# Optimization experiments

Hardware: AMD Instinct MI355X
Metric: run time of the kernel (lower is better)

The kernel has to match this reference:

```python
import jax, jax.numpy as jnp
import numpy as np

N_USERS = 200000
N_ITEMS = 100000
N_NODES = N_USERS + N_ITEMS
N_EDGES = 1500000
EMBED_DIM = 64
BERT_DIM = 384
N_LAYERS = 3


def setup_inputs() -> dict:
    key = jax.random.key(0)
    ks = jax.random.split(key, 13)
    return {
        "user_emb": jax.random.normal(ks[0], (N_USERS, EMBED_DIM), jnp.float32) * 0.1,
        "item_emb": jax.random.normal(ks[1], (N_ITEMS, EMBED_DIM), jnp.float32) * 0.1,
        "gender_emb": jax.random.normal(ks[2], (3, EMBED_DIM), jnp.float32) * 0.1,
        "age_emb": jax.random.normal(ks[3], (8, EMBED_DIM), jnp.float32) * 0.1,
        "cat_emb": jax.random.normal(ks[4], (11, EMBED_DIM), jnp.float32) * 0.1,
        "bert_proj_w": jax.random.normal(ks[5], (EMBED_DIM, BERT_DIM), jnp.float32) * 0.05,
        "item_bert": jax.random.normal(ks[6], (N_ITEMS, BERT_DIM), jnp.float32),
        "adj_val": jax.random.uniform(ks[7], (N_EDGES,), jnp.float32),
        "user_gender": jax.random.randint(ks[8], (N_USERS,), 0, 3, jnp.int64 if jax.config.jax_enable_x64 else jnp.int32),
        "user_age": jax.random.randint(ks[9], (N_USERS,), 0, 8, jnp.int32),
        "item_cat": jax.random.randint(ks[10], (N_ITEMS,), 0, 11, jnp.int32),
        "adj_row": jax.random.randint(ks[11], (N_EDGES,), 0, N_NODES, jnp.int32),
        "adj_col": jax.random.randint(ks[12], (N_EDGES,), 0, N_NODES, jnp.int32),
    }


def reference(user_emb, item_emb, gender_emb, age_emb, cat_emb, bert_proj_w,
              item_bert, adj_val, user_gender, user_age, item_cat,
              adj_row, adj_col):
    n_users = user_emb.shape[0]
    n_nodes = n_users + item_emb.shape[0]

    # initial embeddings: base table + side-info gathers (+ projected BERT for items)
    u0 = user_emb + gender_emb[user_gender] + age_emb[user_age]          # [U, d]
    i0 = item_emb + cat_emb[item_cat] + item_bert @ bert_proj_w.T       # [I, d]
    all_emb = jnp.concatenate([u0, i0], axis=0)                          # [N, d]

    # COO SpMM: y[r] += val * x[c]
    def spmm(x):
        msgs = adj_val[:, None] * x[adj_col]                             # [E, d]
        return jax.ops.segment_sum(msgs, adj_row, num_segments=n_nodes)

    acc = all_emb
    x = all_emb
    for _ in range(N_LAYERS):
        x = spmm(x)
        acc = acc + x
    out = acc / (N_LAYERS + 1)                                           # mean over layer stack
    return out[:n_users], out[n_users:]
```

## Files before the change

### kernel.cpp

```cpp
#include <hip/hip_runtime.h>
#include <hip/hip_bf16.h>

#define NU 200000
#define NI 100000
#define NN 300000
#define NE 1500000
#define BD 384

#define SCAN1_BLOCKS 293
#define NBINS 293
#define CH 4096
#define P2CAP 6144

typedef __attribute__((ext_vector_type(8))) short short8;
typedef __attribute__((ext_vector_type(4))) float floatx4;

__device__ __forceinline__ void fma4(float4& a, float s, const float4& w) {
    a.x = fmaf(s, w.x, a.x);
    a.y = fmaf(s, w.y, a.y);
    a.z = fmaf(s, w.z, a.z);
    a.w = fmaf(s, w.w, a.w);
}

__device__ __forceinline__ float bf2f(unsigned short v) {
    union { unsigned int u; float f; } c; c.u = ((unsigned int)v) << 16; return c.f;
}
__device__ __forceinline__ float4 ub4f(const ushort4 v) {
    return make_float4(bf2f(v.x), bf2f(v.y), bf2f(v.z), bf2f(v.w));
}
__device__ __forceinline__ unsigned short f2bfu(float x) {
    union { __hip_bfloat16 b; unsigned short u; } c; c.b = __float2bfloat16(x); return c.u;
}
__device__ __forceinline__ ushort4 f4bf(const float4 a) {
    return make_ushort4(f2bfu(a.x), f2bfu(a.y), f2bfu(a.z), f2bfu(a.w));
}

__device__ __forceinline__ short8 cvt8(const float4 a, const float4 b) {
    union { short8 v; __hip_bfloat16 e[8]; } u;
    u.e[0] = __float2bfloat16(a.x); u.e[1] = __float2bfloat16(a.y);
    u.e[2] = __float2bfloat16(a.z); u.e[3] = __float2bfloat16(a.w);
    u.e[4] = __float2bfloat16(b.x); u.e[5] = __float2bfloat16(b.y);
    u.e[6] = __float2bfloat16(b.z); u.e[7] = __float2bfloat16(b.w);
    return u.v;
}

__global__ __launch_bounds__(256) void user_init_k(
    const float4* __restrict__ user_emb,
    const float4* __restrict__ gender_emb,
    const float4* __restrict__ age_emb,
    const int* __restrict__ ug,
    const int* __restrict__ ua,
    ushort4* __restrict__ A0)
{
    int i = blockIdx.x * 256 + threadIdx.x;
    int u = i >> 4, q = i & 15;
    float4 e = user_emb[i];
    float4 g = gender_emb[ug[u] * 16 + q];
    float4 a = age_emb[ua[u] * 16 + q];
    e.x += g.x + a.x; e.y += g.y + a.y; e.z += g.z + a.z; e.w += g.w + a.w;
    A0[i] = f4bf(e);
}

__global__ __launch_bounds__(256) void wconv_k(
    const float* __restrict__ W, short8* __restrict__ Wb)
{
    int t = blockIdx.x * 256 + threadIdx.x;
    if (t >= 3072) return;
    int lid = t & 63, nt = (t >> 6) & 3, kt = t >> 8;
    int m16 = lid & 15, q = lid >> 4;
    const float* src = W + (size_t)(nt * 16 + m16) * BD + kt * 32 + q * 8;
    Wb[t] = cvt8(*(const float4*)src, *(const float4*)(src + 4));
}

__global__ __launch_bounds__(256) void item_init_k(
    const float* __restrict__ bert,
    const short8* __restrict__ Wb,
    const float* __restrict__ item_emb,
    const float* __restrict__ cat_emb,
    const int* __restrict__ icat,
    unsigned short* __restrict__ A0)
{
    const int lid = threadIdx.x & 63;
    const int wv  = threadIdx.x >> 6;
    const int i0  = (blockIdx.x * 4 + wv) * 16;
    if (i0 >= NI) return;
    const int m16 = lid & 15;
    const int q   = lid >> 4;

    const float*  ab = bert + (size_t)(i0 + m16) * BD + q * 8;
    const short8* wb = Wb + lid;

    floatx4 cf[4];
    cf[0] = (floatx4){0.f, 0.f, 0.f, 0.f};
    cf[1] = cf[0]; cf[2] = cf[0]; cf[3] = cf[0];

    float4 a0 = *(const float4*)(ab + 0);
    float4 a1 = *(const float4*)(ab + 4);
    short8 b0 = wb[0 * 64];
    short8 b1 = wb[1 * 64];
    short8 b2 = wb[2 * 64];
    short8 b3 = wb[3 * 64];

    #pragma unroll
    for (int kt = 0; kt < 11; ++kt) {
        float4 na0 = *(const float4*)(ab + (kt + 1) * 32 + 0);
        float4 na1 = *(const float4*)(ab + (kt + 1) * 32 + 4);
        short8 nb0 = wb[((kt + 1) * 4 + 0) * 64];
        short8 nb1 = wb[((kt + 1) * 4 + 1) * 64];
        short8 nb2 = wb[((kt + 1) * 4 + 2) * 64];
        short8 nb3 = wb[((kt + 1) * 4 + 3) * 64];
        short8 af = cvt8(a0, a1);
        cf[0] = __builtin_amdgcn_mfma_f32_16x16x32_bf16(af, b0, cf[0], 0, 0, 0);
        cf[1] = __builtin_amdgcn_mfma_f32_16x16x32_bf16(af, b1, cf[1], 0, 0, 0);
        cf[2] = __builtin_amdgcn_mfma_f32_16x16x32_bf16(af, b2, cf[2], 0, 0, 0);
        cf[3] = __builtin_amdgcn_mfma_f32_16x16x32_bf16(af, b3, cf[3], 0, 0, 0);
        a0 = na0; a1 = na1; b0 = nb0; b1 = nb1; b2 = nb2; b3 = nb3;
    }
    {
        short8 af = cvt8(a0, a1);
        cf[0] = __builtin_amdgcn_mfma_f32_16x16x32_bf16(af, b0, cf[0], 0, 0, 0);
        cf[1] = __builtin_amdgcn_mfma_f32_16x16x32_bf16(af, b1, cf[1], 0, 0, 0);
        cf[2] = __builtin_amdgcn_mfma_f32_16x16x32_bf16(af, b2, cf[2], 0, 0, 0);
        cf[3] = __builtin_amdgcn_mfma_f32_16x16x32_bf16(af, b3, cf[3], 0, 0, 0);
    }

    #pragma unroll
    for (int r = 0; r < 4; ++r) {
        const int item = i0 + q * 4 + r;
        const int cat  = icat[item];
        const size_t eb = (size_t)item * 64;
        const size_t abn = (size_t)(NU + item) * 64;
        #pragma unroll
        for (int td = 0; td < 4; ++td) {
            const int d = td * 16 + m16;
            A0[abn + d] = f2bfu(cf[td][r] + item_emb[eb + d] + cat_emb[cat * 64 + d]);
        }
    }
}

__global__ __launch_bounds__(256) void hist_k(
    const int* __restrict__ row, int* __restrict__ counts)
{
    int e = blockIdx.x * 256 + threadIdx.x;
    if (e < NE) atomicAdd(&counts[row[e]], 1);
}

__global__ __launch_bounds__(256) void scan1_k(
    const int* __restrict__ counts, int* __restrict__ offs,
    int* __restrict__ blksum)
{
    __shared__ int s[256];
    int t = threadIdx.x;
    int base = blockIdx.x * 1024 + t * 4;
    int c0 = 0, c1 = 0, c2 = 0, c3 = 0;
    if (base + 3 < NN) {
        int4 c = *(const int4*)&counts[base];
        c0 = c.x; c1 = c.y; c2 = c.z; c3 = c.w;
    } else {
        if (base + 0 < NN) c0 = counts[base + 0];
        if (base + 1 < NN) c1 = counts[base + 1];
        if (base + 2 < NN) c2 = counts[base + 2];
    }
    int tsum = c0 + c1 + c2 + c3;
    s[t] = tsum;
    __syncthreads();
    for (int d = 1; d < 256; d <<= 1) {
        int v = (t >= d) ? s[t - d] : 0;
        __syncthreads();
        s[t] += v;
        __syncthreads();
    }
    if (t == 255) blksum[blockIdx.x] = s[255];
    int e0 = s[t] - tsum, e1 = e0 + c0, e2 = e1 + c1, e3 = e2 + c2;
    if (base + 0 < NN) offs[base + 0] = e0;
    if (base + 1 < NN) offs[base + 1] = e1;
    if (base + 2 < NN) offs[base + 2] = e2;
    if (base + 3 < NN) offs[base + 3] = e3;
}

__global__ __launch_bounds__(512) void scan2_k(int* __restrict__ blksum)
{
    __shared__ int s[512];
    int t = threadIdx.x;
    int v = (t < SCAN1_BLOCKS) ? blksum[t] : 0;
    s[t] = v;
    __syncthreads();
    for (int d = 1; d < 512; d <<= 1) {
        int x = (t >= d) ? s[t - d] : 0;
        __syncthreads();
        s[t] += x;
        __syncthreads();
    }
    if (t < SCAN1_BLOCKS) blksum[t] = s[t] - v;
}

__global__ __launch_bounds__(256) void addoff_k(
    int* __restrict__ offs, const int* __restrict__ blkoff,
    int* __restrict__ cursor,
    int* __restrict__ binstart, int* __restrict__ bincur)
{
    int i = blockIdx.x * 256 + threadIdx.x;
    if (i < NN) {
        int o = offs[i] + blkoff[i >> 10];
        offs[i] = o;
        cursor[i] = o;
        if ((i & 1023) == 0) {
            binstart[i >> 10] = o;
            bincur[i >> 10] = o;
        }
    }
}

__global__ __launch_bounds__(256) void binscat_k(
    const int* __restrict__ row, const int* __restrict__ col,
    const float* __restrict__ val,
    int* __restrict__ bincur,
    int2* __restrict__ tcv, int* __restrict__ trow)
{
    __shared__ int lhist[512];
    __shared__ int lexcl[512];
    __shared__ int lbase[512];
    __shared__ int s[256];
    __shared__ int2 scv[CH];
    __shared__ int  srow[CH];

    int t = threadIdx.x;
    int e0 = blockIdx.x * CH;
    int n = NE - e0; if (n > CH) n = CH;

    lhist[t] = 0; lhist[t + 256] = 0;
    __syncthreads();

    int r[16]; int2 cv[16]; int rk[16];
    #pragma unroll
    for (int i = 0; i < 16; ++i) {
        int idx = e0 + i * 256 + t;
        if (idx < NE) {
            r[i] = row[idx];
            cv[i].x = col[idx];
            cv[i].y = __float_as_int(val[idx]);
            rk[i] = atomicAdd(&lhist[r[i] >> 10], 1);
        }
    }
    __syncthreads();

    int c0 = lhist[2 * t], c1 = lhist[2 * t + 1];
    int tsum = c0 + c1;
    s[t] = tsum;
    __syncthreads();
    for (int d = 1; d < 256; d <<= 1) {
        int v = (t >= d) ? s[t - d] : 0;
        __syncthreads();
        s[t] += v;
        __syncthreads();
    }
    int ex = s[t] - tsum;
    lexcl[2 * t] = ex; lexcl[2 * t + 1] = ex + c0;
    if (2 * t < NBINS && c0 > 0)     lbase[2 * t]     = atomicAdd(&bincur[2 * t], c0);
    if (2 * t + 1 < NBINS && c1 > 0) lbase[2 * t + 1] = atomicAdd(&bincur[2 * t + 1], c1);
    __syncthreads();

    #pragma unroll
    for (int i = 0; i < 16; ++i) {
        int idx = e0 + i * 256 + t;
        if (idx < NE) {
            int b = r[i] >> 10;
            int p = lexcl[b] + rk[i];
            scv[p] = cv[i];
            srow[p] = r[i];
        }
    }
    __syncthreads();

    for (int p = t; p < n; p += 256) {
        int rr = srow[p];
        int b = rr >> 10;
        int g = lbase[b] + (p - lexcl[b]);
        tcv[g] = scv[p];
        trow[g] = rr;
    }
}

__global__ __launch_bounds__(256) void scatter2_k(
    const int2* __restrict__ tcv, const int* __restrict__ trow,
    const int* __restrict__ binstart,
    int* __restrict__ cursor, int2* __restrict__ edges)
{
    __shared__ int2 scv[P2CAP];
    int b = blockIdx.x;
    int s = binstart[b];
    int e = (b + 1 < NBINS) ? binstart[b + 1] : NE;
    int cnt = e - s;

    if (cnt <= P2CAP) {
        for (int p = s + threadIdx.x; p < e; p += 256) {
            int rr = trow[p];
            int pos = atomicAdd(&cursor[rr], 1);
            scv[pos - s] = tcv[p];
        }
        __syncthreads();
        for (int p = threadIdx.x; p < cnt; p += 256)
            edges[s + p] = scv[p];
    } else {
        for (int p = s + threadIdx.x; p < e; p += 256) {
            int rr = trow[p];
            int pos = atomicAdd(&cursor[rr], 1);
            edges[pos] = tcv[p];
        }
    }
}

__global__ __launch_bounds__(256) void spmm_bf_k(
    const ushort4* __restrict__ xb,
    ushort4* __restrict__ yb,
    const int* __restrict__ offs,
    const int* __restrict__ ends,
    const int2* __restrict__ edges)
{
    int t = threadIdx.x;
    int r = blockIdx.x * 16 + (t >> 4);
    int q = t & 15;
    int s = offs[r], e = ends[r];
    float4 acc = make_float4(0.f, 0.f, 0.f, 0.f);
    int k = s;
    for (; k + 4 <= e; k += 4) {
        int2 c0 = edges[k + 0];
        int2 c1 = edges[k + 1];
        int2 c2 = edges[k + 2];
        int2 c3 = edges[k + 3];
        ushort4 v0 = xb[c0.x * 16 + q];
        ushort4 v1 = xb[c1.x * 16 + q];
        ushort4 v2 = xb[c2.x * 16 + q];
        ushort4 v3 = xb[c3.x * 16 + q];
        fma4(acc, __int_as_float(c0.y), ub4f(v0));
        fma4(acc, __int_as_float(c1.y), ub4f(v1));
        fma4(acc, __int_as_float(c2.y), ub4f(v2));
        fma4(acc, __int_as_float(c3.y), ub4f(v3));
    }
    for (; k < e; ++k) {
        int2 cv = edges[k];
        fma4(acc, __int_as_float(cv.y), ub4f(xb[cv.x * 16 + q]));
    }
    yb[r * 16 + q] = f4bf(acc);
}

__global__ __launch_bounds__(256) void spmm_l3_k(
    const ushort4* __restrict__ xb,
    const ushort4* __restrict__ x0b,
    const ushort4* __restrict__ x1b,
    float4* __restrict__ out,
    const int* __restrict__ offs,
    const int* __restrict__ ends,
    const int2* __restrict__ edges)
{
    int t = threadIdx.x;
    int r = blockIdx.x * 16 + (t >> 4);
    int q = t & 15;
    int s = offs[r], e = ends[r];
    float4 acc = make_float4(0.f, 0.f, 0.f, 0.f);
    int k = s;
    for (; k + 4 <= e; k += 4) {
        int2 c0 = edges[k + 0];
        int2 c1 = edges[k + 1];
        int2 c2 = edges[k + 2];
        int2 c3 = edges[k + 3];
        ushort4 v0 = xb[c0.x * 16 + q];
        ushort4 v1 = xb[c1.x * 16 + q];
        ushort4 v2 = xb[c2.x * 16 + q];
        ushort4 v3 = xb[c3.x * 16 + q];
        fma4(acc, __int_as_float(c0.y), ub4f(v0));
        fma4(acc, __int_as_float(c1.y), ub4f(v1));
        fma4(acc, __int_as_float(c2.y), ub4f(v2));
        fma4(acc, __int_as_float(c3.y), ub4f(v3));
    }
    for (; k < e; ++k) {
        int2 cv = edges[k];
        fma4(acc, __int_as_float(cv.y), ub4f(xb[cv.x * 16 + q]));
    }
    int oi = r * 16 + q;
    float4 x0 = ub4f(x0b[oi]);
    float4 x1 = ub4f(x1b[oi]);
    float4 x2 = ub4f(xb[oi]);
    out[oi] = make_float4(0.25f * (x0.x + x1.x + x2.x + acc.x),
                          0.25f * (x0.y + x1.y + x2.y + acc.y),
                          0.25f * (x0.z + x1.z + x2.z + acc.z),
                          0.25f * (x0.w + x1.w + x2.w + acc.w));
}

extern "C" void kernel_launch(void* const* d_in, const int* in_sizes, int n_in,
                              void* d_out, int out_size, void* d_ws, size_t ws_size,
                              hipStream_t stream)
{
    const float* user_emb    = (const float*)d_in[0];
    const float* item_emb    = (const float*)d_in[1];
    const float* gender_emb  = (const float*)d_in[2];
    const float* age_emb     = (const float*)d_in[3];
    const float* cat_emb     = (const float*)d_in[4];
    const float* bert_w      = (const float*)d_in[5];
    const float* item_bert   = (const float*)d_in[6];
    const float* adj_val     = (const float*)d_in[7];
    const int*   user_gender = (const int*)d_in[8];
    const int*   user_age    = (const int*)d_in[9];
    const int*   item_cat    = (const int*)d_in[10];
    const int*   adj_row     = (const int*)d_in[11];
    const int*   adj_col     = (const int*)d_in[12];

    float* out = (float*)d_out;

    float* A       = (float*)d_ws;
    float* B       = A + (size_t)NN * 64;
    int2*  edges   = (int2*)(B + (size_t)NN * 64);
    int*   offs    = (int*)(edges + NE);
    int*   cursor  = offs + NN;
    int*   blksum  = cursor + NN;
    int*   binstart= blksum + 512;
    int*   bincur  = binstart + 512;
    short8* Wb     = (short8*)(bincur + 512);

    ushort4* A0_16 = (ushort4*)A;
    int2*    tcv  = (int2*)B;
    int*     trow = (int*)(tcv + NE);
    ushort4* B16  = (ushort4*)B;
    ushort4* A16  = B16 + (size_t)NN * 16;

    hipMemsetAsync(offs, 0, (size_t)NN * sizeof(int), stream);
    hist_k<<<5860, 256, 0, stream>>>(adj_row, offs);
    scan1_k<<<SCAN1_BLOCKS, 256, 0, stream>>>(offs, offs, blksum);
    scan2_k<<<1, 512, 0, stream>>>(blksum);
    addoff_k<<<1172, 256, 0, stream>>>(offs, blksum, cursor, binstart, bincur);
    binscat_k<<<367, 256, 0, stream>>>(adj_row, adj_col, adj_val, bincur, tcv, trow);
    scatter2_k<<<NBINS, 256, 0, stream>>>(tcv, trow, binstart, cursor, edges);

    wconv_k<<<12, 256, 0, stream>>>(bert_w, Wb);
    user_init_k<<<12500, 256, 0, stream>>>(
        (const float4*)user_emb, (const float4*)gender_emb, (const float4*)age_emb,
        user_gender, user_age, A0_16);
    item_init_k<<<1563, 256, 0, stream>>>(
        item_bert, Wb, item_emb, cat_emb, item_cat, (unsigned short*)A0_16);

    spmm_bf_k<<<18750, 256, 0, stream>>>(A0_16, B16, offs, cursor, edges);
    spmm_bf_k<<<18750, 256, 0, stream>>>(B16, A16, offs, cursor, edges);
    spmm_l3_k<<<18750, 256, 0, stream>>>(A16, A0_16, B16, (float4*)out,
                                         offs, cursor, edges);
}
```

Measured before the change: 624.2 us.

## Pack row-in-bin into column bits and split item projection K across wave pairs

The binned edge scatter now stores each row's low 10 bits in the upper bits of the column index. This drops the separate trow array and its global write and read, and shrinks shared staging from int rows to ushort bins. Separately, the item BERT projection splits the 384-wide K dimension across two waves per 16-item tile and reduces their partial results through shared memory, doubling the wave count to raise memory-level parallelism. The trade-offs are an extra __syncthreads plus LDS traffic, and the bit packing depends on column indices fitting in 19 bits.

```diff
diff --git a/kernel.cpp b/kernel.cpp
--- a/kernel.cpp
+++ b/kernel.cpp
@@ -11,6 +11,7 @@
 #define NBINS 293
 #define CH 4096
 #define P2CAP 6144
+#define COLMASK 0x7FFFF
 
 typedef __attribute__((ext_vector_type(8))) short short8;
 typedef __attribute__((ext_vector_type(4))) float floatx4;
@@ -80,15 +81,18 @@
     const int* __restrict__ icat,
     unsigned short* __restrict__ A0)
 {
-    const int lid = threadIdx.x & 63;
-    const int wv  = threadIdx.x >> 6;
-    const int i0  = (blockIdx.x * 4 + wv) * 16;
-    if (i0 >= NI) return;
-    const int m16 = lid & 15;
-    const int q   = lid >> 4;
-
-    const float*  ab = bert + (size_t)(i0 + m16) * BD + q * 8;
-    const short8* wb = Wb + lid;
+    __shared__ float4 cbuf[2][4][64];
+
+    const int lid  = threadIdx.x & 63;
+    const int wv   = threadIdx.x >> 6;
+    const int pair = wv >> 1;
+    const int kh   = wv & 1;
+    const int i0   = (blockIdx.x * 2 + pair) * 16;
+    const int m16  = lid & 15;
+    const int q    = lid >> 4;
+
+    const float*  ab = bert + (size_t)(i0 + m16) * BD + kh * 192 + q * 8;
+    const short8* wb = Wb + kh * 24 * 64 + lid;
 
     floatx4 cf[4];
     cf[0] = (floatx4){0.f, 0.f, 0.f, 0.f};
@@ -102,7 +106,7 @@
     short8 b3 = wb[3 * 64];
 
     #pragma unroll
-    for (int kt = 0; kt < 11; ++kt) {
+    for (int kt = 0; kt < 5; ++kt) {
         float4 na0 = *(const float4*)(ab + (kt + 1) * 32 + 0);
         float4 na1 = *(const float4*)(ab + (kt + 1) * 32 + 4);
         short8 nb0 = wb[((kt + 1) * 4 + 0) * 64];
@@ -124,6 +128,20 @@
         cf[3] = __builtin_amdgcn_mfma_f32_16x16x32_bf16(af, b3, cf[3], 0, 0, 0);
     }
 
+    if (kh == 1) {
+        #pragma unroll
+        for (int f = 0; f < 4; ++f)
+            cbuf[pair][f][lid] = make_float4(cf[f][0], cf[f][1], cf[f][2], cf[f][3]);
+    }
+    __syncthreads();
+    if (kh == 1) return;
+
+    #pragma unroll
+    for (int f = 0; f < 4; ++f) {
+        float4 p = cbuf[pair][f][lid];
+        cf[f][0] += p.x; cf[f][1] += p.y; cf[f][2] += p.z; cf[f][3] += p.w;
+    }
+
     #pragma unroll
     for (int r = 0; r < 4; ++r) {
         const int item = i0 + q * 4 + r;
@@ -215,14 +233,14 @@
     const int* __restrict__ row, const int* __restrict__ col,
     const float* __restrict__ val,
     int* __restrict__ bincur,
-    int2* __restrict__ tcv, int* __restrict__ trow)
+    int2* __restrict__ tcv)
 {
     __shared__ int lhist[512];
     __shared__ int lexcl[512];
     __shared__ int lbase[512];
     __shared__ int s[256];
     __shared__ int2 scv[CH];
-    __shared__ int  srow[CH];
+    __shared__ unsigned short sbin[CH];
 
     int t = threadIdx.x;
     int e0 = blockIdx.x * CH;
@@ -237,7 +255,7 @@
         int idx = e0 + i * 256 + t;
         if (idx < NE) {
             r[i] = row[idx];
-            cv[i].x = col[idx];
+            cv[i].x = col[idx] | ((r[i] & 1023) << 19);
             cv[i].y = __float_as_int(val[idx]);
             rk[i] = atomicAdd(&lhist[r[i] >> 10], 1);
         }
@@ -267,45 +285,46 @@
             int b = r[i] >> 10;
             int p = lexcl[b] + rk[i];
             scv[p] = cv[i];
-            srow[p] = r[i];
+            sbin[p] = (unsigned short)b;
         }
     }
     __syncthreads();
 
     for (int p = t; p < n; p += 256) {
-        int rr = srow[p];
-        int b = rr >> 10;
+        int b = sbin[p];
         int g = lbase[b] + (p - lexcl[b]);
         tcv[g] = scv[p];
-        trow[g] = rr;
     }
 }
 
 __global__ __launch_bounds__(256) void scatter2_k(
-    const int2* __restrict__ tcv, const int* __restrict__ trow,
+    const int2* __restrict__ tcv,
     const int* __restrict__ binstart,
     int* __restrict__ cursor, int2* __restrict__ edges)
 {
     __shared__ int2 scv[P2CAP];
     int b = blockIdx.x;
+    int rbase = b << 10;
     int s = binstart[b];
     int e = (b + 1 < NBINS) ? binstart[b + 1] : NE;
     int cnt = e - s;
 
     if (cnt <= P2CAP) {
         for (int p = s + threadIdx.x; p < e; p += 256) {
-            int rr = trow[p];
+            int2 tv = tcv[p];
+            int rr = rbase + (int)(((unsigned int)tv.x) >> 19);
             int pos = atomicAdd(&cursor[rr], 1);
-            scv[pos - s] = tcv[p];
+            scv[pos - s] = make_int2(tv.x & COLMASK, tv.y);
         }
         __syncthreads();
         for (int p = threadIdx.x; p < cnt; p += 256)
             edges[s + p] = scv[p];
     } else {
         for (int p = s + threadIdx.x; p < e; p += 256) {
-            int rr = trow[p];
+            int2 tv = tcv[p];
+            int rr = rbase + (int)(((unsigned int)tv.x) >> 19);
             int pos = atomicAdd(&cursor[rr], 1);
-            edges[pos] = tcv[p];
+            edges[pos] = make_int2(tv.x & COLMASK, tv.y);
         }
     }
 }
@@ -419,7 +438,6 @@
 
     ushort4* A0_16 = (ushort4*)A;
     int2*    tcv  = (int2*)B;
-    int*     trow = (int*)(tcv + NE);
     ushort4* B16  = (ushort4*)B;
     ushort4* A16  = B16 + (size_t)NN * 16;
 
@@ -428,14 +446,14 @@
     scan1_k<<<SCAN1_BLOCKS, 256, 0, stream>>>(offs, offs, blksum);
     scan2_k<<<1, 512, 0, stream>>>(blksum);
     addoff_k<<<1172, 256, 0, stream>>>(offs, blksum, cursor, binstart, bincur);
-    binscat_k<<<367, 256, 0, stream>>>(adj_row, adj_col, adj_val, bincur, tcv, trow);
-    scatter2_k<<<NBINS, 256, 0, stream>>>(tcv, trow, binstart, cursor, edges);
+    binscat_k<<<367, 256, 0, stream>>>(adj_row, adj_col, adj_val, bincur, tcv);
+    scatter2_k<<<NBINS, 256, 0, stream>>>(tcv, binstart, cursor, edges);
 
     wconv_k<<<12, 256, 0, stream>>>(bert_w, Wb);
     user_init_k<<<12500, 256, 0, stream>>>(
         (const float4*)user_emb, (const float4*)gender_emb, (const float4*)age_emb,
         user_gender, user_age, A0_16);
-    item_init_k<<<1563, 256, 0, stream>>>(
+    item_init_k<<<3125, 256, 0, stream>>>(
         item_bert, Wb, item_emb, cat_emb, item_cat, (unsigned short*)A0_16);
 
     spmm_bf_k<<<18750, 256, 0, stream>>>(A0_16, B16, offs, cursor, edges);
```

Result: no change. 618.0 us (-1.0%).
